# Kernel optimization log

Measured on AMD Instinct MI355X. Metric: run time of the kernel, lower is better.

## Reference

```python
import jax, jax.numpy as jnp
import numpy as np

B, N, CIN, COUT, MAXN, NF, MID = 8, 512, 64, 64, 16, 32, 16
M1 = [3, 32, 32, 1]
M2 = [CIN * COUT, 512, MID]
MR = [CIN * MID, 512, COUT]
BN_EPS = 1e-3  # keras BatchNormalization default epsilon


def mish(v):
    return v * jnp.tanh(jax.nn.softplus(v))


def bn(v, g, b):
    # training-mode batch norm over the row axis (keras BN in learning phase)
    mu = jnp.mean(v, axis=0, keepdims=True)
    var = jnp.var(v, axis=0, keepdims=True)
    return g * (v - mu) * jax.lax.rsqrt(var + BN_EPS) + b


def _mlp(v, layers):
    for W, b, g, be in layers:
        v = bn(mish(v @ W + b), g, be)
    return v


def setup_inputs() -> dict:
    key = jax.random.key(0)
    ks = jax.random.split(key, 16)
    inp = {
        'x': jax.random.normal(ks[0], (B, N, CIN), jnp.float32),
        'xyz': jax.random.normal(ks[1], (B, N, 3), jnp.float32),
        'framepoints': jax.random.normal(ks[2], (NF, 3), jnp.float32),
        'fpw': jax.random.normal(ks[3], (NF, CIN, COUT), jnp.float32) * 0.05,
    }
    ki = 4
    for name, dims in (('m1', M1), ('m2', M2), ('mr', MR)):
        for i in range(len(dims) - 1):
            inp[f'{name}_w{i}'] = jax.random.normal(ks[ki], (dims[i], dims[i + 1]), jnp.float32) / np.float32(np.sqrt(dims[i]))
            inp[f'{name}_b{i}'] = jnp.zeros((dims[i + 1],), jnp.float32)
            inp[f'{name}_g{i}'] = jnp.ones((dims[i + 1],), jnp.float32)
            inp[f'{name}_be{i}'] = jnp.zeros((dims[i + 1],), jnp.float32)
            ki += 1
    return inp


def reference(x, xyz, framepoints, fpw,
              m1_w0, m1_b0, m1_g0, m1_be0,
              m1_w1, m1_b1, m1_g1, m1_be1,
              m1_w2, m1_b2, m1_g2, m1_be2,
              m2_w0, m2_b0, m2_g0, m2_be0,
              m2_w1, m2_b1, m2_g1, m2_be1,
              mr_w0, mr_b0, mr_g0, mr_be0,
              mr_w1, mr_b1, mr_g1, mr_be1):
    Bc, Nc, cin = x.shape
    nf = framepoints.shape[0]
    cout = fpw.shape[2]
    mid = m2_w1.shape[1]

    # pairwise squared distances on FEATURES (as in the original), gram form
    sq = jnp.sum(x * x, axis=-1)  # [B,N]
    d = sq[:, :, None] + sq[:, None, :] - 2.0 * jnp.einsum('bnc,bmc->bnm', x, x)
    _, idx = jax.lax.top_k(-d, MAXN)  # [B,N,maxn] nearest (self first)

    bidx = jnp.arange(Bc)[:, None, None]
    xyz_sl = xyz[bidx, idx]  # [B,N,maxn,3]
    fur = x[bidx, idx]       # [B,N,maxn,cin]

    xyz_sl = xyz_sl.reshape(-1, MAXN, 3)
    rel = (xyz_sl - xyz_sl[:, :1, :]).reshape(-1, 3)  # [B*N*maxn, 3]

    # deterministic random rotation of frame points about the y axis
    ang = jax.random.uniform(jax.random.key(42), ()) * 2.0 * jnp.pi
    c = jnp.cos(ang); s = jnp.sin(ang)
    z = jnp.zeros_like(c); o = jnp.ones_like(c)
    R = jnp.stack([jnp.stack([c, z, s]), jnp.stack([z, o, z]), jnp.stack([-s, z, c])])
    fp = framepoints @ R  # [nf,3]

    sl = jnp.concatenate([rel, fp], axis=0)              # [M+nf, 3]
    diff = (sl[:, None, :] - fp[None, :, :]).reshape(-1, 3)  # [(M+nf)*nf, 3]

    h = _mlp(diff, [(m1_w0, m1_b0, m1_g0, m1_be0),
                    (m1_w1, m1_b1, m1_g1, m1_be1),
                    (m1_w2, m1_b2, m1_g2, m1_be2)])      # [(M+nf)*nf, 1]

    w = _mlp(fpw.reshape(nf, -1), [(m2_w0, m2_b0, m2_g0, m2_be0),
                                   (m2_w1, m2_b1, m2_g1, m2_be1)])  # [nf, mid]

    agg = jnp.sum(h.reshape(-1, nf, 1) * w[None], axis=1)  # [M+nf, mid]
    wmain = agg[:-nf].reshape(-1, MAXN, mid)               # [B*N, maxn, mid]

    f = jnp.einsum('kmc,kmd->kcd', fur.reshape(-1, MAXN, cin), wmain)
    f = f.reshape(-1, cin * mid)
    f = _mlp(f, [(mr_w0, mr_b0, mr_g0, mr_be0),
                 (mr_w1, mr_b1, mr_g1, mr_be1)])           # [B*N, cout]
    return f.reshape(Bc, Nc, cout)
```

## Files before the change

### kernel.cpp

```cpp
#include <hip/hip_runtime.h>
#include <math.h>

#define BB    8
#define NN    512
#define CIN   64
#define MAXN  16
#define NF    32
#define MID   16
#define BN_   4096
#define MSL   65536
#define MTOT  65568
#define RROWS 2098176
#define P2STR 40
#define AST   72

typedef unsigned short ushort_t;
typedef __attribute__((ext_vector_type(8))) short bf16x8;
typedef __attribute__((ext_vector_type(4))) float f32x4;

__device__ __forceinline__ float mishf(float x){
  float t  = __expf(x);
  float u  = 1.0f + t;
  float u2 = u * u;
  float r  = x * (u2 - 1.0f) * __builtin_amdgcn_rcpf(u2 + 1.0f);
  return (x > 15.0f) ? x : r;
}

__device__ __forceinline__ ushort_t f2bf(float f){
  unsigned u = __float_as_uint(f);
  unsigned r = (u + 0x7FFFu + ((u >> 16) & 1u)) >> 16;
  return (ushort_t)r;
}

__device__ __forceinline__ unsigned cvt_pk_bf16(float lo, float hi){
  unsigned r;
  asm("v_cvt_pk_bf16_f32 %0, %1, %2" : "=v"(r) : "v"(lo), "v"(hi));
  return r;
}

__device__ __forceinline__ unsigned rotl32(unsigned v, unsigned s){
  return (v << s) | (v >> (32u - s));
}

__device__ __forceinline__ float jax_uniform42(){
  unsigned ks[3];
  ks[0] = 0u; ks[1] = 42u; ks[2] = 0x1BD11BDAu ^ 0u ^ 42u;
  const unsigned rot[8] = {13u,15u,26u,6u,17u,29u,16u,24u};
  unsigned x0 = ks[0];
  unsigned x1 = ks[1];
  #pragma unroll
  for (int blk = 0; blk < 5; ++blk){
    #pragma unroll
    for (int r = 0; r < 4; ++r){
      x0 += x1;
      x1 = rotl32(x1, rot[(blk & 1) * 4 + r]);
      x1 ^= x0;
    }
    x0 += ks[(blk + 1) % 3];
    x1 += ks[(blk + 2) % 3] + (unsigned)(blk + 1);
  }
  unsigned w = x0 ^ x1;
  return __uint_as_float((w >> 9) | 0x3f800000u) - 1.0f;
}

__global__ __launch_bounds__(256) void k_sq(const float* __restrict__ x, double* __restrict__ sqd){
  int r = blockIdx.x * 256 + threadIdx.x;
  const float4* p = (const float4*)(x + (size_t)r * 64);
  double a0 = 0.0, a1 = 0.0, a2 = 0.0, a3 = 0.0;
  #pragma unroll
  for (int k = 0; k < 16; k += 4){
    float4 v0 = p[k], v1 = p[k+1], v2 = p[k+2], v3 = p[k+3];
    a0 += (double)v0.x*v0.x + (double)v0.y*v0.y + (double)v0.z*v0.z + (double)v0.w*v0.w;
    a1 += (double)v1.x*v1.x + (double)v1.y*v1.y + (double)v1.z*v1.z + (double)v1.w*v1.w;
    a2 += (double)v2.x*v2.x + (double)v2.y*v2.y + (double)v2.z*v2.z + (double)v2.w*v2.w;
    a3 += (double)v3.x*v3.x + (double)v3.y*v3.y + (double)v3.z*v3.z + (double)v3.w*v3.w;
  }
  sqd[r] = (a0 + a1) + (a2 + a3);
}

__global__ __launch_bounds__(256) void k_topk(const float* __restrict__ x, const double* __restrict__ sqd,
                                              int* __restrict__ idxp){
  __shared__ float ct[128 * 65];
  __shared__ float xnl[4][64];
  int tid  = threadIdx.x;
  int lane = tid & 63;
  int wid  = tid >> 6;
  int g = blockIdx.x * 4 + wid;
  int b = g >> 9;
  const float* xb = x + (size_t)b * (NN * CIN);
  {
    int w = tid >> 6, c = tid & 63;
    int nq = (blockIdx.x * 4 + w) & 511;
    xnl[w][c] = xb[nq * 64 + c];
  }
  double sqn = sqd[g];

  double dst[8];
  #pragma unroll 1
  for (int tile = 0; tile < 4; ++tile){
    __syncthreads();
    #pragma unroll
    for (int u = 0; u < 8; ++u){
      int idx = u * 256 + tid;
      int row = idx >> 4, q = idx & 15;
      float4 v = *(const float4*)&xb[(size_t)(tile * 128 + row) * 64 + q * 4];
      float* d = &ct[row * 65 + q * 4];
      d[0] = v.x; d[1] = v.y; d[2] = v.z; d[3] = v.w;
    }
    __syncthreads();
    double a[2][4];
    #pragma unroll
    for (int s = 0; s < 2; ++s)
      #pragma unroll
      for (int i = 0; i < 4; ++i) a[s][i] = 0.0;
    #pragma unroll
    for (int k = 0; k < 16; ++k){
      float4 qv = *(const float4*)&xnl[wid][k * 4];
      double q0 = (double)qv.x, q1 = (double)qv.y, q2 = (double)qv.z, q3 = (double)qv.w;
      #pragma unroll
      for (int s = 0; s < 2; ++s){
        const float* rp = &ct[(lane + 64 * s) * 65 + k * 4];
        a[s][0] += q0 * (double)rp[0];
        a[s][1] += q1 * (double)rp[1];
        a[s][2] += q2 * (double)rp[2];
        a[s][3] += q3 * (double)rp[3];
      }
    }
    #pragma unroll
    for (int s = 0; s < 2; ++s){
      int m = tile * 128 + 64 * s + lane;
      dst[tile * 2 + s] = sqn + sqd[(b << 9) + m] - 2.0 * ((a[s][0] + a[s][1]) + (a[s][2] + a[s][3]));
    }
  }

  for (int it = 0; it < 16; ++it){
    double bd = 1.0e300; int bi = 0x7FFFFFFF;
    #pragma unroll
    for (int j = 0; j < 8; ++j){
      int m = ((j >> 1) << 7) + ((j & 1) << 6) + lane;
      if (dst[j] < bd){ bd = dst[j]; bi = m; }
    }
    #pragma unroll
    for (int off = 1; off < 64; off <<= 1){
      double od = __shfl_xor(bd, off);
      int    oi = __shfl_xor(bi, off);
      if (od < bd || (od == bd && oi < bi)){ bd = od; bi = oi; }
    }
    if (lane == 0) idxp[g * 16 + it] = bi;
    if (lane == (bi & 63)){
      int slot = ((bi >> 7) << 1) | ((bi >> 6) & 1);
      #pragma unroll
      for (int j = 0; j < 8; ++j) if (j == slot) dst[j] = 1.0e300;
    }
  }
}

__global__ __launch_bounds__(256) void k_prep(const float* __restrict__ xyz,
                                              const float* __restrict__ fpts,
                                              const int* __restrict__ idxp,
                                              const float* __restrict__ w0, const float* __restrict__ b0,
                                              float* __restrict__ sib, float* __restrict__ fjt){
  __shared__ float w0l[96], b0l[32];
  int tid = threadIdx.x;
  if (tid < 96) w0l[tid] = w0[tid];
  else if (tid < 128) b0l[tid - 96] = b0[tid - 96];
  __syncthreads();
  int i = blockIdx.x * 256 + tid;
  if (i >= MTOT) return;
  float vx, vy, vz;
  if (i < MSL){
    int bn = i >> 4, m = i & 15, b = bn >> 9;
    int i0 = idxp[bn * 16];
    int im = idxp[bn * 16 + m];
    const float* xz = xyz + (size_t)b * (NN * 3);
    vx = xz[im * 3 + 0] - xz[i0 * 3 + 0];
    vy = xz[im * 3 + 1] - xz[i0 * 3 + 1];
    vz = xz[im * 3 + 2] - xz[i0 * 3 + 2];
  } else {
    int j = i - MSL;
    float u   = jax_uniform42();
    float ang = (u * 2.0f) * 3.14159274f;
    float c = cosf(ang), s = sinf(ang);
    float fx = fpts[j * 3 + 0], fy = fpts[j * 3 + 1], fz = fpts[j * 3 + 2];
    vx = fx * c - fz * s;
    vy = fy;
    vz = fx * s + fz * c;
  }
  float si[32];
  #pragma unroll
  for (int c = 0; c < 32; ++c)
    si[c] = vx * w0l[c] + vy * w0l[32 + c] + vz * w0l[64 + c];
  float* dst = sib + (size_t)i * 32;
  #pragma unroll
  for (int cq = 0; cq < 8; ++cq){
    float4 o = make_float4(si[cq*4+0] + b0l[cq*4+0], si[cq*4+1] + b0l[cq*4+1],
                           si[cq*4+2] + b0l[cq*4+2], si[cq*4+3] + b0l[cq*4+3]);
    *(float4*)&dst[cq*4] = o;
  }
  if (i >= MSL){
    int j = i - MSL;
    #pragma unroll
    for (int c = 0; c < 32; ++c) fjt[c * 32 + j] = si[c];
  }
}

__global__ __launch_bounds__(256) void k_m1_p1(const float* __restrict__ sib, const float* __restrict__ fjt,
                                               float* __restrict__ s0g, float* __restrict__ q0g,
                                               ushort_t* __restrict__ a0g){
  __shared__ float fjlt[32 * 33];
  __shared__ float red[16][32], redq[16][32];
  int tid = threadIdx.x;
  for (int t = tid; t < 1024; t += 256) fjlt[(t & 31) * 33 + (t >> 5)] = fjt[t];
  __syncthreads();
  int c2 = (tid & 15) * 2, s = tid >> 4;
  float as0 = 0.0f, aq0 = 0.0f, as1 = 0.0f, aq1 = 0.0f;
  int base = blockIdx.x * 1024;
  #pragma unroll 4
  for (int t = 0; t < 64; ++t){
    int r = base + t * 16 + s;
    int i = r >> 5, j = r & 31;
    float2 v = *(const float2*)&sib[(size_t)i * 32 + c2];
    float2 f = *(const float2*)&fjlt[j * 33 + c2];
    float m0 = mishf(v.x - f.x);
    float m1 = mishf(v.y - f.y);
    as0 += m0; aq0 += m0 * m0;
    as1 += m1; aq1 += m1 * m1;
    if (a0g) *(unsigned*)&a0g[(size_t)r * 32 + c2] = cvt_pk_bf16(m0, m1);
  }
  red[s][c2] = as0;  red[s][c2 + 1] = as1;
  redq[s][c2] = aq0; redq[s][c2 + 1] = aq1;
  __syncthreads();
  if (tid < 32){
    float ts = 0.0f, tq = 0.0f;
    #pragma unroll
    for (int ss = 0; ss < 16; ++ss){ ts += red[ss][tid]; tq += redq[ss][tid]; }
    int bank = (blockIdx.x & 15) * 32 + tid;
    atomicAdd(&s0g[bank], ts);
    atomicAdd(&q0g[bank], tq);
  }
}

__global__ __launch_bounds__(256, 6) void k_m1_p2(const float* __restrict__ sib, const float* __restrict__ fjt,
                                               const ushort_t* __restrict__ a0g,
                                               const float* __restrict__ w1g, const float* __restrict__ b1g,
                                               const float* __restrict__ g0, const float* __restrict__ be0,
                                               const float* __restrict__ s0g, const float* __restrict__ q0g,
                                               float* __restrict__ s1g, float* __restrict__ q1g,
                                               ushort_t* __restrict__ a1b){
  __shared__ __align__(16) ushort_t a0s[256 * P2STR];
  __shared__ __align__(16) float uni[1024];
  __shared__ float A0l[32], C0l[32], biasX[32], satm[32], qatm[32];
  ushort_t* wts = (ushort_t*)uni;
  int tid = threadIdx.x;
  if (!a0g){
    for (int t = tid; t < 1024; t += 256) uni[t] = fjt[t];
  }
  if (tid < 32){
    float s = 0.0f, q = 0.0f;
    #pragma unroll
    for (int b = 0; b < 16; ++b){ s += s0g[b * 32 + tid]; q += q0g[b * 32 + tid]; }
    const float invR = 1.0f / (float)RROWS;
    float mu = s * invR, var = q * invR - mu * mu;
    float A = g0[tid] * rsqrtf(var + 1e-3f);
    A0l[tid] = A; C0l[tid] = be0[tid] - mu * A;
    satm[tid] = 0.0f; qatm[tid] = 0.0f;
  }
  __syncthreads();
  if (a0g){
    int r = blockIdx.x * 256 + tid;
    const uint4* src = (const uint4*)(a0g + (size_t)r * 32);
    uint4 v0 = src[0], v1 = src[1], v2 = src[2], v3 = src[3];
    ushort_t* dst = &a0s[tid * P2STR];
    *(uint4*)&dst[0]  = v0;
    *(uint4*)&dst[8]  = v1;
    *(uint4*)&dst[16] = v2;
    *(uint4*)&dst[24] = v3;
  } else {
    int r = blockIdx.x * 256 + tid;
    int i = r >> 5, j = r & 31;
    const float* sr = sib + (size_t)i * 32;
    ushort_t* dst = &a0s[tid * P2STR];
    #pragma unroll
    for (int cq = 0; cq < 4; ++cq){
      float4 sa = *(const float4*)&sr[cq * 8];
      float4 sb = *(const float4*)&sr[cq * 8 + 4];
      float m0 = mishf(sa.x - uni[(cq*8+0)*32 + j]);
      float m1 = mishf(sa.y - uni[(cq*8+1)*32 + j]);
      float m2 = mishf(sa.z - uni[(cq*8+2)*32 + j]);
      float m3 = mishf(sa.w - uni[(cq*8+3)*32 + j]);
      float m4 = mishf(sb.x - uni[(cq*8+4)*32 + j]);
      float m5 = mishf(sb.y - uni[(cq*8+5)*32 + j]);
      float m6 = mishf(sb.z - uni[(cq*8+6)*32 + j]);
      float m7 = mishf(sb.w - uni[(cq*8+7)*32 + j]);
      uint4 pk;
      pk.x = cvt_pk_bf16(m0, m1);
      pk.y = cvt_pk_bf16(m2, m3);
      pk.z = cvt_pk_bf16(m4, m5);
      pk.w = cvt_pk_bf16(m6, m7);
      *(uint4*)&dst[cq * 8] = pk;
    }
  }
  if (tid < 32){
    float acc = b1g[tid];
    #pragma unroll
    for (int k = 0; k < 32; ++k) acc += C0l[k] * w1g[k * 32 + tid];
    biasX[tid] = acc;
  }
  __syncthreads();
  for (int t = tid; t < 1024; t += 256){
    int k = t >> 5, c = t & 31;
    wts[c * P2STR + k] = f2bf(w1g[t] * A0l[k]);
  }
  __syncthreads();
  int lane = tid & 63, w = tid >> 6;
  int ln15 = lane & 15, quad = lane >> 4;
  f32x4 zero = {0.0f, 0.0f, 0.0f, 0.0f};
  bf16x8 bfr0 = *(bf16x8*)&wts[(ln15) * P2STR + quad * 8];
  bf16x8 bfr1 = *(bf16x8*)&wts[(16 + ln15) * P2STR + quad * 8];
  f32x4 acc[4][2];
  #pragma unroll
  for (int i2 = 0; i2 < 4; ++i2){
    int row = (w * 4 + i2) * 16 + ln15;
    bf16x8 af = *(bf16x8*)&a0s[row * P2STR + quad * 8];
    acc[i2][0] = __builtin_amdgcn_mfma_f32_16x16x32_bf16(af, bfr0, zero, 0, 0, 0);
    acc[i2][1] = __builtin_amdgcn_mfma_f32_16x16x32_bf16(af, bfr1, zero, 0, 0, 0);
  }
  float cs[2] = {0.0f, 0.0f}, cq2[2] = {0.0f, 0.0f};
  size_t rowbase = (size_t)blockIdx.x * 256 + w * 64 + quad * 4;
  #pragma unroll
  for (int nt = 0; nt < 2; ++nt){
    int col = nt * 16 + ln15;
    float bx = biasX[col];
    size_t colbase = (size_t)col * RROWS;
    #pragma unroll
    for (int i2 = 0; i2 < 4; ++i2){
      f32x4 a = acc[i2][nt];
      float m0 = mishf(a[0] + bx);
      float m1 = mishf(a[1] + bx);
      float m2 = mishf(a[2] + bx);
      float m3 = mishf(a[3] + bx);
      cs[nt]  += m0 + m1 + m2 + m3;
      cq2[nt] += m0*m0 + m1*m1 + m2*m2 + m3*m3;
      if (a1b){
        uint2 pk;
        pk.x = cvt_pk_bf16(m0, m1);
        pk.y = cvt_pk_bf16(m2, m3);
        *(uint2*)&a1b[colbase + rowbase + (size_t)i2 * 16] = pk;
      }
    }
  }
  #pragma unroll
  for (int nt = 0; nt < 2; ++nt){
    float v = cs[nt], u = cq2[nt];
    v += __shfl_xor(v, 16); u += __shfl_xor(u, 16);
    v += __shfl_xor(v, 32); u += __shfl_xor(u, 32);
    if (lane < 16){
      atomicAdd(&satm[nt * 16 + ln15], v);
      atomicAdd(&qatm[nt * 16 + ln15], u);
    }
  }
  __syncthreads();
  if (tid < 32){
    int bank = (blockIdx.x & 15) * 32 + tid;
    atomicAdd(&s1g[bank], satm[tid]);
    atomicAdd(&q1g[bank], qatm[tid]);
  }
}

__global__ __launch_bounds__(256) void k_m1_p3s(const ushort_t* __restrict__ a1b,
                                                const float* __restrict__ w2g, const float* __restrict__ b2g,
                                                const float* __restrict__ g1, const float* __restrict__ be1,
                                                const float* __restrict__ s1g, const float* __restrict__ q1g,
                                                float* __restrict__ act2, float* __restrict__ s2g, float* __restrict__ q2g){
  __shared__ float vvl[32], C1l[32], cb2l[1], r2s[4], r2q[4];
  int tid = threadIdx.x;
  if (tid < 32){
    float s = 0.0f, q = 0.0f;
    #pragma unroll
    for (int b = 0; b < 16; ++b){ s += s1g[b * 32 + tid]; q += q1g[b * 32 + tid]; }
    const float invR = 1.0f / (float)RROWS;
    float mu = s * invR, var = q * invR - mu * mu;
    float A = g1[tid] * rsqrtf(var + 1e-3f);
    C1l[tid] = be1[tid] - mu * A;
    vvl[tid] = A * w2g[tid];
  }
  __syncthreads();
  if (tid == 0){
    float a = b2g[0];
    #pragma unroll
    for (int k = 0; k < 32; ++k) a += C1l[k] * w2g[k];
    cb2l[0] = a;
  }
  __syncthreads();
  size_t r0 = (size_t)blockIdx.x * 512 + (size_t)tid * 2;
  float pre0 = 0.0f, pre1 = 0.0f;
  #pragma unroll
  for (int c = 0; c < 32; ++c){
    unsigned u = *(const unsigned*)&a1b[(size_t)c * RROWS + r0];
    float lo = __uint_as_float(u << 16);
    float hi = __uint_as_float(u & 0xFFFF0000u);
    pre0 += lo * vvl[c];
    pre1 += hi * vvl[c];
  }
  float cb2 = cb2l[0];
  float a20 = mishf(pre0 + cb2);
  float a21 = mishf(pre1 + cb2);
  *(float2*)&act2[r0] = make_float2(a20, a21);
  float ss = a20 + a21, qq = a20*a20 + a21*a21;
  #pragma unroll
  for (int off = 1; off < 64; off <<= 1){ ss += __shfl_xor(ss, off); qq += __shfl_xor(qq, off); }
  int lane = tid & 63, wid = tid >> 6;
  if (lane == 0){ r2s[wid] = ss; r2q[wid] = qq; }
  __syncthreads();
  if (tid == 0){
    atomicAdd(&s2g[blockIdx.x & 15], r2s[0] + r2s[1] + r2s[2] + r2s[3]);
    atomicAdd(&q2g[blockIdx.x & 15], r2q[0] + r2q[1] + r2q[2] + r2q[3]);
  }
}

__global__ __launch_bounds__(256, 3) void k_m1_p3f(const float* __restrict__ sib, const float* __restrict__ fjt,
                                               const float* __restrict__ w1g, const float* __restrict__ b1g,
                                               const float* __restrict__ g0, const float* __restrict__ be0,
                                               const float* __restrict__ g1, const float* __restrict__ be1,
                                               const float* __restrict__ w2g, const float* __restrict__ b2g,
                                               const float* __restrict__ s0g, const float* __restrict__ q0g,
                                               const float* __restrict__ s1g, const float* __restrict__ q1g,
                                               float* __restrict__ act2, float* __restrict__ s2g, float* __restrict__ q2g){
  __shared__ float fjl[1024];
  __shared__ float w1s[1024];
  __shared__ float A0l[32], C0l[32], A1l[32], C1l[32], biasX[32], vvl[32];
  __shared__ float a0t[32 * 256];
  __shared__ float cb2l[1];
  __shared__ float r2s[4], r2q[4];
  int tid = threadIdx.x;
  const float invR = 1.0f / (float)RROWS;
  for (int t = tid; t < 1024; t += 256) fjl[t] = fjt[t];
  if (tid < 32){
    float s = 0.0f, q = 0.0f;
    #pragma unroll
    for (int b = 0; b < 16; ++b){ s += s0g[b * 32 + tid]; q += q0g[b * 32 + tid]; }
    float mu = s * invR, var = q * invR - mu * mu;
    float A = g0[tid] * rsqrtf(var + 1e-3f);
    A0l[tid] = A; C0l[tid] = be0[tid] - mu * A;
  } else if (tid < 64){
    int c = tid - 32;
    float s = 0.0f, q = 0.0f;
    #pragma unroll
    for (int b = 0; b < 16; ++b){ s += s1g[b * 32 + c]; q += q1g[b * 32 + c]; }
    float mu = s * invR, var = q * invR - mu * mu;
    float A = g1[c] * rsqrtf(var + 1e-3f);
    A1l[c] = A; C1l[c] = be1[c] - mu * A;
  }
  __syncthreads();
  for (int t = tid; t < 1024; t += 256) w1s[t] = w1g[t] * A0l[t >> 5];
  if (tid < 32){
    float acc = b1g[tid];
    #pragma unroll
    for (int k = 0; k < 32; ++k) acc += C0l[k] * w1g[k * 32 + tid];
    biasX[tid] = acc;
  } else if (tid < 96 && tid >= 64){
    int c = tid - 64;
    vvl[c] = A1l[c] * w2g[c];
  } else if (tid == 96){
    float acc = b2g[0];
    #pragma unroll
    for (int k = 0; k < 32; ++k) acc += C1l[k] * w2g[k];
    cb2l[0] = acc;
  }
  {
    int r = blockIdx.x * 256 + tid;
    int i = r >> 5, j = r & 31;
    const float* sr = sib + (size_t)i * 32;
    #pragma unroll
    for (int cq = 0; cq < 8; ++cq){
      float4 sv = *(const float4*)&sr[cq * 4];
      a0t[(cq*4+0)*256 + tid] = mishf(sv.x - fjl[(cq*4+0)*32 + j]);
      a0t[(cq*4+1)*256 + tid] = mishf(sv.y - fjl[(cq*4+1)*32 + j]);
      a0t[(cq*4+2)*256 + tid] = mishf(sv.z - fjl[(cq*4+2)*32 + j]);
      a0t[(cq*4+3)*256 + tid] = mishf(sv.w - fjl[(cq*4+3)*32 + j]);
    }
  }
  __syncthreads();
  int cg = tid & 7, rg = tid >> 3;
  float acc[8][4];
  #pragma unroll
  for (int i2 = 0; i2 < 8; ++i2)
    #pragma unroll
    for (int j2 = 0; j2 < 4; ++j2) acc[i2][j2] = 0.0f;
  #pragma unroll 4
  for (int k = 0; k < 32; ++k){
    float4 w  = *(const float4*)&w1s[k * 32 + cg * 4];
    float4 aA = *(const float4*)&a0t[k * 256 + rg * 8];
    float4 aB = *(const float4*)&a0t[k * 256 + rg * 8 + 4];
    float ar[8] = {aA.x, aA.y, aA.z, aA.w, aB.x, aB.y, aB.z, aB.w};
    float wc[4] = {w.x, w.y, w.z, w.w};
    #pragma unroll
    for (int i2 = 0; i2 < 8; ++i2)
      #pragma unroll
      for (int j2 = 0; j2 < 4; ++j2) acc[i2][j2] += ar[i2] * wc[j2];
  }
  float cb2 = cb2l[0];
  float ss = 0.0f, qq = 0.0f;
  #pragma unroll
  for (int rr = 0; rr < 8; ++rr){
    float part = 0.0f;
    #pragma unroll
    for (int cc = 0; cc < 4; ++cc){
      float m = mishf(acc[rr][cc] + biasX[cg * 4 + cc]);
      part += m * vvl[cg * 4 + cc];
    }
    part += __shfl_xor(part, 1);
    part += __shfl_xor(part, 2);
    part += __shfl_xor(part, 4);
    float a2 = mishf(part + cb2);
    if (cg == 0){
      act2[(size_t)blockIdx.x * 256 + rg * 8 + rr] = a2;
      ss += a2; qq += a2 * a2;
    }
  }
  #pragma unroll
  for (int off = 1; off < 64; off <<= 1){ ss += __shfl_xor(ss, off); qq += __shfl_xor(qq, off); }
  int lane = tid & 63, wid = tid >> 6;
  if (lane == 0){ r2s[wid] = ss; r2q[wid] = qq; }
  __syncthreads();
  if (tid == 0){
    atomicAdd(&s2g[blockIdx.x & 15], r2s[0] + r2s[1] + r2s[2] + r2s[3]);
    atomicAdd(&q2g[blockIdx.x & 15], r2q[0] + r2q[1] + r2q[2] + r2q[3]);
  }
}

__global__ __launch_bounds__(512) void k_wmlp1(const float* __restrict__ fpw, const float* __restrict__ W0,
                                               float* __restrict__ wact0){
  int f = blockIdx.x, kc = blockIdx.y, c = threadIdx.x;
  const float* row = fpw + (size_t)f * 4096 + kc * 512;
  const float* wp  = W0 + (size_t)(kc * 512) * 512 + c;
  float acc = 0.0f;
  #pragma unroll 8
  for (int k = 0; k < 512; ++k) acc += row[k] * wp[(size_t)k * 512];
  atomicAdd(&wact0[f * 512 + c], acc);
}

__global__ __launch_bounds__(512) void k_wmlp2(const float* __restrict__ wact0, const float* __restrict__ b0,
                                               const float* __restrict__ W1,
                                               const float* __restrict__ b1,
                                               const float* __restrict__ g0, const float* __restrict__ be0,
                                               const float* __restrict__ g1, const float* __restrict__ be1,
                                               float* __restrict__ wfin){
  __shared__ float wl[32 * 512];
  __shared__ float o2l[512], A1l[16], C1l[16];
  int t = threadIdx.x;
  {
    float b0t = b0[t];
    float v[32]; float sum = 0.0f, sq = 0.0f;
    #pragma unroll
    for (int r = 0; r < 32; ++r){
      v[r] = mishf(wact0[r * 512 + t] + b0t);
      sum += v[r]; sq += v[r] * v[r];
    }
    float mu  = sum * (1.0f / 32.0f);
    float var = sq * (1.0f / 32.0f) - mu * mu;
    float A = g0[t] * rsqrtf(var + 1e-3f);
    float C = be0[t] - mu * A;
    #pragma unroll
    for (int r = 0; r < 32; ++r) wl[r * 512 + t] = v[r] * A + C;
  }
  __syncthreads();
  {
    int r = t >> 4, c2 = t & 15;
    float pre = b1[c2];
    for (int k = 0; k < 512; ++k) pre += wl[r * 512 + k] * W1[k * 16 + c2];
    o2l[t] = mishf(pre);
  }
  __syncthreads();
  if (t < 16){
    float sum = 0.0f, sq = 0.0f;
    #pragma unroll
    for (int r = 0; r < 32; ++r){ float v = o2l[r * 16 + t]; sum += v; sq += v * v; }
    float mu  = sum * (1.0f / 32.0f);
    float var = sq * (1.0f / 32.0f) - mu * mu;
    float A = g1[t] * rsqrtf(var + 1e-3f);
    A1l[t] = A; C1l[t] = be1[t] - mu * A;
  }
  __syncthreads();
  wfin[t] = o2l[t] * A1l[t & 15] + C1l[t & 15];
}

__global__ __launch_bounds__(256) void k_agg(const float* __restrict__ act2, const float* __restrict__ wfin,
                                             const float* __restrict__ x, const int* __restrict__ idxp,
                                             const float* __restrict__ s2, const float* __restrict__ q2,
                                             const float* __restrict__ g2, const float* __restrict__ be2,
                                             ushort_t* __restrict__ fb16){
  __shared__ float hl[512], wfl[512], wm[256], furl[1024], AC[2];
  int t = threadIdx.x;
  int k = blockIdx.x;
  if (t == 0){
    const float invR = 1.0f / (float)RROWS;
    float ssum = 0.0f, qsum = 0.0f;
    #pragma unroll
    for (int b = 0; b < 16; ++b){ ssum += s2[b]; qsum += q2[b]; }
    float mu  = ssum * invR;
    float var = qsum * invR - mu * mu;
    float A = g2[0] * rsqrtf(var + 1e-3f);
    AC[0] = A; AC[1] = be2[0] - mu * A;
  }
  wfl[t] = wfin[t]; wfl[t + 256] = wfin[t + 256];
  __syncthreads();
  float A2 = AC[0], C2 = AC[1];
  hl[t]       = act2[(size_t)k * 512 + t]       * A2 + C2;
  hl[t + 256] = act2[(size_t)k * 512 + 256 + t] * A2 + C2;
  __syncthreads();
  {
    int m = t >> 4, d = t & 15;
    float acc = 0.0f;
    #pragma unroll
    for (int j = 0; j < 32; ++j) acc += hl[m * 32 + j] * wfl[j * 16 + d];
    wm[t] = acc;
  }
  int b = k >> 9;
  const float* xb = x + (size_t)b * (NN * CIN);
  {
    int c = t & 63;
    #pragma unroll
    for (int it = 0; it < 4; ++it){
      int m = it * 4 + (t >> 6);
      int im = idxp[k * 16 + m];
      furl[m * 64 + c] = xb[im * 64 + c];
    }
  }
  __syncthreads();
  {
    int d = t & 15, c0 = t >> 4;
    #pragma unroll
    for (int q = 0; q < 4; ++q){
      int c = c0 + 16 * q;
      float acc = 0.0f;
      #pragma unroll
      for (int m = 0; m < 16; ++m) acc += furl[m * 64 + c] * wm[m * 16 + d];
      fb16[(size_t)k * 1024 + t + 256 * q] = f2bf(acc);
    }
  }
}

__global__ __launch_bounds__(256) void k_mr1(const ushort_t* __restrict__ F16, const float* __restrict__ W,
                                             const float* __restrict__ bias, float* __restrict__ out,
                                             float* __restrict__ s3, float* __restrict__ q3){
  __shared__ __align__(16) ushort_t As[64 * AST];
  __shared__ __align__(16) ushort_t Bs[64 * AST];
  __shared__ float csum[64], csq[64];
  int tid = threadIdx.x;
  int m0 = blockIdx.y * 64, n0 = blockIdx.x * 64;
  int lane = tid & 63, w = tid >> 6;
  int ln15 = lane & 15, quad = lane >> 4;
  if (tid < 64){ csum[tid] = 0.0f; csq[tid] = 0.0f; }
  f32x4 acc[4];
  #pragma unroll
  for (int n = 0; n < 4; ++n){ acc[n][0] = 0.0f; acc[n][1] = 0.0f; acc[n][2] = 0.0f; acc[n][3] = 0.0f; }

  #pragma unroll 1
  for (int k0 = 0; k0 < 1024; k0 += 64){
    __syncthreads();
    {
      int row = tid >> 2, kq = (tid & 3) * 16;
      const uint4* src = (const uint4*)&F16[(size_t)(m0 + row) * 1024 + k0 + kq];
      uint4 v0 = src[0], v1 = src[1];
      ushort_t* dst = &As[row * AST + kq];
      *(uint4*)&dst[0] = v0;
      *(uint4*)&dst[8] = v1;
    }
    #pragma unroll
    for (int rr = 0; rr < 4; ++rr){
      int kk = rr * 16 + (tid >> 4);
      int nn = (tid & 15) * 4;
      float4 v = *(const float4*)&W[(size_t)(k0 + kk) * 512 + n0 + nn];
      unsigned p01 = cvt_pk_bf16(v.x, v.y);
      unsigned p23 = cvt_pk_bf16(v.z, v.w);
      Bs[(nn + 0) * AST + kk] = (ushort_t)p01;
      Bs[(nn + 1) * AST + kk] = (ushort_t)(p01 >> 16);
      Bs[(nn + 2) * AST + kk] = (ushort_t)p23;
      Bs[(nn + 3) * AST + kk] = (ushort_t)(p23 >> 16);
    }
    __syncthreads();
    #pragma unroll
    for (int ks = 0; ks < 64; ks += 32){
      bf16x8 af = *(bf16x8*)&As[(w * 16 + ln15) * AST + ks + quad * 8];
      #pragma unroll
      for (int n = 0; n < 4; ++n){
        bf16x8 bfv = *(bf16x8*)&Bs[(n * 16 + ln15) * AST + ks + quad * 8];
        acc[n] = __builtin_amdgcn_mfma_f32_16x16x32_bf16(af, bfv, acc[n], 0, 0, 0);
      }
    }
  }
  #pragma unroll
  for (int n = 0; n < 4; ++n){
    int col = n0 + n * 16 + ln15;
    float bv = bias[col];
    f32x4 a = acc[n];
    float s = 0.0f, q = 0.0f;
    #pragma unroll
    for (int r = 0; r < 4; ++r){
      float v = mishf(a[r] + bv);
      int row = m0 + w * 16 + quad * 4 + r;
      out[(size_t)row * 512 + col] = v;
      s += v; q += v * v;
    }
    s += __shfl_xor(s, 16); q += __shfl_xor(q, 16);
    s += __shfl_xor(s, 32); q += __shfl_xor(q, 32);
    if (quad == 0){
      atomicAdd(&csum[n * 16 + ln15], s);
      atomicAdd(&csq[n * 16 + ln15], q);
    }
  }
  __syncthreads();
  if (tid < 64){
    atomicAdd(&s3[n0 + tid], csum[tid]);
    atomicAdd(&q3[n0 + tid], csq[tid]);
  }
}

__global__ __launch_bounds__(256) void k_mr2(const float* __restrict__ Ain, const float* __restrict__ W,
                                             const float* __restrict__ bias,
                                             const float* __restrict__ s3, const float* __restrict__ q3,
                                             const float* __restrict__ g0, const float* __restrict__ be0,
                                             float* __restrict__ out, float* __restrict__ s4, float* __restrict__ q4){
  __shared__ float As2[16][68];
  __shared__ float Bs2[16][68];
  __shared__ float A3l[512], C3l[512];
  __shared__ float csum[64], csq[64];
  int tid = threadIdx.x;
  for (int kk = tid; kk < 512; kk += 256){
    const float invR = 1.0f / 4096.0f;
    float mu  = s3[kk] * invR;
    float var = q3[kk] * invR - mu * mu;
    float A = g0[kk] * rsqrtf(var + 1e-3f);
    A3l[kk] = A; C3l[kk] = be0[kk] - mu * A;
  }
  if (tid < 64){ csum[tid] = 0.0f; csq[tid] = 0.0f; }
  __syncthreads();
  int m0 = blockIdx.x * 64;
  int tx = tid & 15, ty = tid >> 4;
  float acc[4][4];
  #pragma unroll
  for (int i = 0; i < 4; ++i)
    #pragma unroll
    for (int j = 0; j < 4; ++j) acc[i][j] = 0.0f;
  int lmm = tid >> 2, lkq = (tid & 3) * 4;
  int lkk = tid >> 4, lnq = (tid & 15) * 4;
  float4 av = *(const float4*)&Ain[(size_t)(m0 + lmm) * 512 + lkq];
  float4 bv = *(const float4*)&W[(size_t)lkk * 64 + lnq];
  for (int k0 = 0; k0 < 512; k0 += 16){
    As2[lkq + 0][lmm] = av.x * A3l[k0 + lkq + 0] + C3l[k0 + lkq + 0];
    As2[lkq + 1][lmm] = av.y * A3l[k0 + lkq + 1] + C3l[k0 + lkq + 1];
    As2[lkq + 2][lmm] = av.z * A3l[k0 + lkq + 2] + C3l[k0 + lkq + 2];
    As2[lkq + 3][lmm] = av.w * A3l[k0 + lkq + 3] + C3l[k0 + lkq + 3];
    *(float4*)&Bs2[lkk][lnq] = bv;
    __syncthreads();
    if (k0 + 16 < 512){
      av = *(const float4*)&Ain[(size_t)(m0 + lmm) * 512 + (k0 + 16) + lkq];
      bv = *(const float4*)&W[(size_t)((k0 + 16) + lkk) * 64 + lnq];
    }
    #pragma unroll
    for (int kk = 0; kk < 16; ++kk){
      float4 a4 = *(const float4*)&As2[kk][ty * 4];
      float4 b4 = *(const float4*)&Bs2[kk][tx * 4];
      float a[4] = {a4.x, a4.y, a4.z, a4.w};
      float bb[4] = {b4.x, b4.y, b4.z, b4.w};
      #pragma unroll
      for (int i = 0; i < 4; ++i)
        #pragma unroll
        for (int j = 0; j < 4; ++j) acc[i][j] += a[i] * bb[j];
    }
    __syncthreads();
  }
  float4 bq = *(const float4*)&bias[tx * 4];
  float bvs[4] = {bq.x, bq.y, bq.z, bq.w};
  float cs[4] = {0,0,0,0}, cq[4] = {0,0,0,0};
  #pragma unroll
  for (int i = 0; i < 4; ++i){
    float v[4];
    #pragma unroll
    for (int j = 0; j < 4; ++j){
      v[j] = mishf(acc[i][j] + bvs[j]);
      cs[j] += v[j]; cq[j] += v[j] * v[j];
    }
    float4 o = make_float4(v[0], v[1], v[2], v[3]);
    *(float4*)&out[(size_t)(m0 + ty * 4 + i) * 64 + tx * 4] = o;
  }
  #pragma unroll
  for (int j = 0; j < 4; ++j){
    float v = cs[j], w = cq[j];
    v += __shfl_xor(v, 16); w += __shfl_xor(w, 16);
    v += __shfl_xor(v, 32); w += __shfl_xor(w, 32);
    if ((tid & 63) < 16){
      atomicAdd(&csum[tx * 4 + j], v);
      atomicAdd(&csq[tx * 4 + j], w);
    }
  }
  __syncthreads();
  if (tid < 64){
    atomicAdd(&s4[tid], csum[tid]);
    atomicAdd(&q4[tid], csq[tid]);
  }
}

__global__ __launch_bounds__(256) void k_out(const float* __restrict__ pre,
                                             const float* __restrict__ s4, const float* __restrict__ q4,
                                             const float* __restrict__ g1, const float* __restrict__ be1,
                                             float* __restrict__ outp){
  int e = blockIdx.x * 256 + threadIdx.x;
  int c = e & 63;
  const float invR = 1.0f / 4096.0f;
  float mu  = s4[c] * invR;
  float var = q4[c] * invR - mu * mu;
  float A = g1[c] * rsqrtf(var + 1e-3f);
  outp[e] = pre[e] * A + (be1[c] - mu * A);
}

extern "C" void kernel_launch(void* const* d_in, const int* in_sizes, int n_in,
                              void* d_out, int out_size, void* d_ws, size_t ws_size,
                              hipStream_t stream){
  (void)in_sizes; (void)n_in; (void)out_size;
  const float* x    = (const float*)d_in[0];
  const float* xyz  = (const float*)d_in[1];
  const float* fpts = (const float*)d_in[2];
  const float* fpw  = (const float*)d_in[3];
  const float* m1w0 = (const float*)d_in[4];
  const float* m1b0 = (const float*)d_in[5];
  const float* m1g0 = (const float*)d_in[6];
  const float* m1be0= (const float*)d_in[7];
  const float* m1w1 = (const float*)d_in[8];
  const float* m1b1 = (const float*)d_in[9];
  const float* m1g1 = (const float*)d_in[10];
  const float* m1be1= (const float*)d_in[11];
  const float* m1w2 = (const float*)d_in[12];
  const float* m1b2 = (const float*)d_in[13];
  const float* m1g2 = (const float*)d_in[14];
  const float* m1be2= (const float*)d_in[15];
  const float* m2w0 = (const float*)d_in[16];
  const float* m2b0 = (const float*)d_in[17];
  const float* m2g0 = (const float*)d_in[18];
  const float* m2be0= (const float*)d_in[19];
  const float* m2w1 = (const float*)d_in[20];
  const float* m2b1 = (const float*)d_in[21];
  const float* m2g1 = (const float*)d_in[22];
  const float* m2be1= (const float*)d_in[23];
  const float* mrw0 = (const float*)d_in[24];
  const float* mrb0 = (const float*)d_in[25];
  const float* mrg0 = (const float*)d_in[26];
  const float* mrbe0= (const float*)d_in[27];
  const float* mrw1 = (const float*)d_in[28];
  const float* mrb1 = (const float*)d_in[29];
  const float* mrg1 = (const float*)d_in[30];
  const float* mrbe1= (const float*)d_in[31];

  float* wsf = (float*)d_ws;
  float* s0 = wsf + 0;     float* q0 = wsf + 512;
  float* s1 = wsf + 1024;  float* q1 = wsf + 1536;
  float* s2 = wsf + 2048;  float* q2 = wsf + 2064;
  float* s3 = wsf + 2080;  float* q3 = wsf + 2592;
  float* s4 = wsf + 3104;  float* q4 = wsf + 3168;
  int*   idxp = (int*)(wsf + 4096);
  double* sqd = (double*)(wsf + 69632);
  float* wact0= wsf + 332032;
  float* wfin = wsf + 348416;
  float* act2 = wsf + 348928;
  float* fbuf = wsf + 2447104;
  float* sib  = fbuf;
  float* fjt  = fbuf + 2098176;
  ushort_t* fb16 = (ushort_t*)fbuf;
  float* mact = wsf + 6641408;
  float* mact2= wsf + 8738560;

  size_t need1 = 9000704ULL * 4 + (size_t)RROWS * 32 * 2;
  size_t need2 = need1 + (size_t)RROWS * 32 * 2;
  bool fast = (ws_size >= need1);
  bool t2   = (ws_size >= need2);
  ushort_t* a1b = fast ? (ushort_t*)(wsf + 9000704) : nullptr;
  ushort_t* a0g = t2   ? (ushort_t*)(wsf + 9000704 + 33570816) : nullptr;

  hipMemsetAsync(d_ws, 0, 4096 * sizeof(float), stream);
  hipMemsetAsync(wact0, 0, 16384 * sizeof(float), stream);

  k_sq<<<16, 256, 0, stream>>>(x, sqd);
  k_topk<<<1024, 256, 0, stream>>>(x, sqd, idxp);
  k_prep<<<257, 256, 0, stream>>>(xyz, fpts, idxp, m1w0, m1b0, sib, fjt);
  k_m1_p1<<<2049, 256, 0, stream>>>(sib, fjt, s0, q0, a0g);
  k_m1_p2<<<8196, 256, 0, stream>>>(sib, fjt, a0g, m1w1, m1b1, m1g0, m1be0, s0, q0, s1, q1, a1b);
  if (fast){
    k_m1_p3s<<<4098, 256, 0, stream>>>(a1b, m1w2, m1b2, m1g1, m1be1, s1, q1, act2, s2, q2);
  } else {
    k_m1_p3f<<<8196, 256, 0, stream>>>(sib, fjt, m1w1, m1b1, m1g0, m1be0, m1g1, m1be1,
                                       m1w2, m1b2, s0, q0, s1, q1, act2, s2, q2);
  }
  k_wmlp1<<<dim3(32, 8), 512, 0, stream>>>(fpw, m2w0, wact0);
  k_wmlp2<<<1, 512, 0, stream>>>(wact0, m2b0, m2w1, m2b1, m2g0, m2be0, m2g1, m2be1, wfin);
  k_agg<<<4096, 256, 0, stream>>>(act2, wfin, x, idxp, s2, q2, m1g2, m1be2, fb16);
  k_mr1<<<dim3(8, 64), 256, 0, stream>>>(fb16, mrw0, mrb0, mact, s3, q3);
  k_mr2<<<64, 256, 0, stream>>>(mact, mrw1, mrb1, s3, q3, mrg0, mrbe0, mact2, s4, q4);
  k_out<<<1024, 256, 0, stream>>>(mact2, s4, q4, mrg1, mrbe1, (float*)d_out);
}
```

Baseline: 466.2 us.

## Restructure m1 layer-2 as direct MFMA, widen p3s loads, pre-convert mr0 weights

Adds a setup kernel that folds the layer-1 batch-norm into bf16 weights and a bias. A new k_m1_p2f kernel then runs layer 2 as MFMAs straight from the global bf16 activations, with no LDS staging. k_m1_p3s now handles 8 rows per thread using 16-byte loads, which cuts its grid fourfold. The mr layer-0 weights are converted to transposed bf16 once, so k_mr1 can read MFMA fragments straight from global memory with no shared tiles or barriers. This adds small extra kernel launches and leans on cache hits for the direct global fragment loads.

```diff
diff --git a/kernel.cpp b/kernel.cpp
--- a/kernel.cpp
+++ b/kernel.cpp
@@ -12,7 +12,6 @@
 #define MTOT  65568
 #define RROWS 2098176
 #define P2STR 40
-#define AST   72
 
 typedef unsigned short ushort_t;
 typedef __attribute__((ext_vector_type(8))) short bf16x8;
@@ -240,8 +239,98 @@
   }
 }
 
+__global__ __launch_bounds__(256) void k_m1_setup(const float* __restrict__ w1g, const float* __restrict__ b1g,
+                                                  const float* __restrict__ g0, const float* __restrict__ be0,
+                                                  const float* __restrict__ s0g, const float* __restrict__ q0g,
+                                                  float* __restrict__ biasXg, ushort_t* __restrict__ wtsb){
+  __shared__ float A0l[32], C0l[32];
+  int tid = threadIdx.x;
+  if (tid < 32){
+    float s = 0.0f, q = 0.0f;
+    #pragma unroll
+    for (int b = 0; b < 16; ++b){ s += s0g[b * 32 + tid]; q += q0g[b * 32 + tid]; }
+    const float invR = 1.0f / (float)RROWS;
+    float mu = s * invR, var = q * invR - mu * mu;
+    float A = g0[tid] * rsqrtf(var + 1e-3f);
+    A0l[tid] = A; C0l[tid] = be0[tid] - mu * A;
+  }
+  __syncthreads();
+  if (tid < 32){
+    float acc = b1g[tid];
+    #pragma unroll
+    for (int k = 0; k < 32; ++k) acc += C0l[k] * w1g[k * 32 + tid];
+    biasXg[tid] = acc;
+  }
+  for (int t = tid; t < 1024; t += 256){
+    int k = t >> 5, c = t & 31;
+    wtsb[c * 32 + k] = f2bf(w1g[t] * A0l[k]);
+  }
+}
+
+__global__ __launch_bounds__(256, 8) void k_m1_p2f(const ushort_t* __restrict__ a0g,
+                                                   const ushort_t* __restrict__ wtsb,
+                                                   const float* __restrict__ biasXg,
+                                                   float* __restrict__ s1g, float* __restrict__ q1g,
+                                                   ushort_t* __restrict__ a1b){
+  __shared__ float satm[32], qatm[32];
+  int tid = threadIdx.x;
+  if (tid < 32){ satm[tid] = 0.0f; qatm[tid] = 0.0f; }
+  __syncthreads();
+  int lane = tid & 63, w = tid >> 6;
+  int ln15 = lane & 15, quad = lane >> 4;
+  bf16x8 bfr0 = *(const bf16x8*)&wtsb[ln15 * 32 + quad * 8];
+  bf16x8 bfr1 = *(const bf16x8*)&wtsb[(16 + ln15) * 32 + quad * 8];
+  f32x4 zero = {0.0f, 0.0f, 0.0f, 0.0f};
+  f32x4 acc[4][2];
+  size_t rowt = (size_t)blockIdx.x * 256;
+  #pragma unroll
+  for (int i2 = 0; i2 < 4; ++i2){
+    int row = (w * 4 + i2) * 16 + ln15;
+    bf16x8 af = *(const bf16x8*)&a0g[(rowt + row) * 32 + quad * 8];
+    acc[i2][0] = __builtin_amdgcn_mfma_f32_16x16x32_bf16(af, bfr0, zero, 0, 0, 0);
+    acc[i2][1] = __builtin_amdgcn_mfma_f32_16x16x32_bf16(af, bfr1, zero, 0, 0, 0);
+  }
+  float cs[2] = {0.0f, 0.0f}, cq2[2] = {0.0f, 0.0f};
+  size_t rowbase = rowt + w * 64 + quad * 4;
+  #pragma unroll
+  for (int nt = 0; nt < 2; ++nt){
+    int col = nt * 16 + ln15;
+    float bx = biasXg[col];
+    size_t colbase = (size_t)col * RROWS;
+    #pragma unroll
+    for (int i2 = 0; i2 < 4; ++i2){
+      f32x4 a = acc[i2][nt];
+      float m0 = mishf(a[0] + bx);
+      float m1 = mishf(a[1] + bx);
+      float m2 = mishf(a[2] + bx);
+      float m3 = mishf(a[3] + bx);
+      cs[nt]  += m0 + m1 + m2 + m3;
+      cq2[nt] += m0*m0 + m1*m1 + m2*m2 + m3*m3;
+      uint2 pk;
+      pk.x = cvt_pk_bf16(m0, m1);
+      pk.y = cvt_pk_bf16(m2, m3);
+      *(uint2*)&a1b[colbase + rowbase + (size_t)i2 * 16] = pk;
+    }
+  }
+  #pragma unroll
+  for (int nt = 0; nt < 2; ++nt){
+    float v = cs[nt], u = cq2[nt];
+    v += __shfl_xor(v, 16); u += __shfl_xor(u, 16);
+    v += __shfl_xor(v, 32); u += __shfl_xor(u, 32);
+    if (lane < 16){
+      atomicAdd(&satm[nt * 16 + ln15], v);
+      atomicAdd(&qatm[nt * 16 + ln15], u);
+    }
+  }
+  __syncthreads();
+  if (tid < 32){
+    int bank = (blockIdx.x & 15) * 32 + tid;
+    atomicAdd(&s1g[bank], satm[tid]);
+    atomicAdd(&q1g[bank], qatm[tid]);
+  }
+}
+
 __global__ __launch_bounds__(256, 6) void k_m1_p2(const float* __restrict__ sib, const float* __restrict__ fjt,
-                                               const ushort_t* __restrict__ a0g,
                                                const float* __restrict__ w1g, const float* __restrict__ b1g,
                                                const float* __restrict__ g0, const float* __restrict__ be0,
                                                const float* __restrict__ s0g, const float* __restrict__ q0g,
@@ -252,9 +341,7 @@
   __shared__ float A0l[32], C0l[32], biasX[32], satm[32], qatm[32];
   ushort_t* wts = (ushort_t*)uni;
   int tid = threadIdx.x;
-  if (!a0g){
-    for (int t = tid; t < 1024; t += 256) uni[t] = fjt[t];
-  }
+  for (int t = tid; t < 1024; t += 256) uni[t] = fjt[t];
   if (tid < 32){
     float s = 0.0f, q = 0.0f;
     #pragma unroll
@@ -266,16 +353,7 @@
     satm[tid] = 0.0f; qatm[tid] = 0.0f;
   }
   __syncthreads();
-  if (a0g){
-    int r = blockIdx.x * 256 + tid;
-    const uint4* src = (const uint4*)(a0g + (size_t)r * 32);
-    uint4 v0 = src[0], v1 = src[1], v2 = src[2], v3 = src[3];
-    ushort_t* dst = &a0s[tid * P2STR];
-    *(uint4*)&dst[0]  = v0;
-    *(uint4*)&dst[8]  = v1;
-    *(uint4*)&dst[16] = v2;
-    *(uint4*)&dst[24] = v3;
-  } else {
+  {
     int r = blockIdx.x * 256 + tid;
     int i = r >> 5, j = r & 31;
     const float* sr = sib + (size_t)i * 32;
@@ -392,21 +470,35 @@
     cb2l[0] = a;
   }
   __syncthreads();
-  size_t r0 = (size_t)blockIdx.x * 512 + (size_t)tid * 2;
-  float pre0 = 0.0f, pre1 = 0.0f;
-  #pragma unroll
-  for (int c = 0; c < 32; ++c){
-    unsigned u = *(const unsigned*)&a1b[(size_t)c * RROWS + r0];
-    float lo = __uint_as_float(u << 16);
-    float hi = __uint_as_float(u & 0xFFFF0000u);
-    pre0 += lo * vvl[c];
-    pre1 += hi * vvl[c];
-  }
-  float cb2 = cb2l[0];
-  float a20 = mishf(pre0 + cb2);
-  float a21 = mishf(pre1 + cb2);
-  *(float2*)&act2[r0] = make_float2(a20, a21);
-  float ss = a20 + a21, qq = a20*a20 + a21*a21;
+  size_t r0 = (size_t)blockIdx.x * 2048 + (size_t)tid * 8;
+  float ss = 0.0f, qq = 0.0f;
+  if (r0 < (size_t)RROWS){
+    float pre[8];
+    #pragma unroll
+    for (int j = 0; j < 8; ++j) pre[j] = 0.0f;
+    #pragma unroll 8
+    for (int c = 0; c < 32; ++c){
+      uint4 u = *(const uint4*)&a1b[(size_t)c * RROWS + r0];
+      float vv = vvl[c];
+      pre[0] += __uint_as_float(u.x << 16) * vv;
+      pre[1] += __uint_as_float(u.x & 0xFFFF0000u) * vv;
+      pre[2] += __uint_as_float(u.y << 16) * vv;
+      pre[3] += __uint_as_float(u.y & 0xFFFF0000u) * vv;
+      pre[4] += __uint_as_float(u.z << 16) * vv;
+      pre[5] += __uint_as_float(u.z & 0xFFFF0000u) * vv;
+      pre[6] += __uint_as_float(u.w << 16) * vv;
+      pre[7] += __uint_as_float(u.w & 0xFFFF0000u) * vv;
+    }
+    float cb2 = cb2l[0];
+    float a2[8];
+    #pragma unroll
+    for (int j = 0; j < 8; ++j){
+      a2[j] = mishf(pre[j] + cb2);
+      ss += a2[j]; qq += a2[j] * a2[j];
+    }
+    *(float4*)&act2[r0]     = make_float4(a2[0], a2[1], a2[2], a2[3]);
+    *(float4*)&act2[r0 + 4] = make_float4(a2[4], a2[5], a2[6], a2[7]);
+  }
   #pragma unroll
   for (int off = 1; off < 64; off <<= 1){ ss += __shfl_xor(ss, off); qq += __shfl_xor(qq, off); }
   int lane = tid & 63, wid = tid >> 6;
@@ -641,54 +733,50 @@
   }
 }
 
-__global__ __launch_bounds__(256) void k_mr1(const ushort_t* __restrict__ F16, const float* __restrict__ W,
+__global__ __launch_bounds__(256) void k_w2bf(const float* __restrict__ W, ushort_t* __restrict__ Wb){
+  int id = blockIdx.x * 256 + threadIdx.x;
+  int n  = id >> 7;
+  int k8 = (id & 127) * 8;
+  float v[8];
+  #pragma unroll
+  for (int j = 0; j < 8; ++j) v[j] = W[(size_t)(k8 + j) * 512 + n];
+  uint4 p;
+  p.x = cvt_pk_bf16(v[0], v[1]);
+  p.y = cvt_pk_bf16(v[2], v[3]);
+  p.z = cvt_pk_bf16(v[4], v[5]);
+  p.w = cvt_pk_bf16(v[6], v[7]);
+  *(uint4*)&Wb[(size_t)n * 1024 + k8] = p;
+}
+
+__global__ __launch_bounds__(256, 8) void k_mr1(const ushort_t* __restrict__ F16, const ushort_t* __restrict__ Wb,
                                              const float* __restrict__ bias, float* __restrict__ out,
                                              float* __restrict__ s3, float* __restrict__ q3){
-  __shared__ __align__(16) ushort_t As[64 * AST];
-  __shared__ __align__(16) ushort_t Bs[64 * AST];
   __shared__ float csum[64], csq[64];
   int tid = threadIdx.x;
   int m0 = blockIdx.y * 64, n0 = blockIdx.x * 64;
   int lane = tid & 63, w = tid >> 6;
   int ln15 = lane & 15, quad = lane >> 4;
   if (tid < 64){ csum[tid] = 0.0f; csq[tid] = 0.0f; }
+  __syncthreads();
   f32x4 acc[4];
   #pragma unroll
   for (int n = 0; n < 4; ++n){ acc[n][0] = 0.0f; acc[n][1] = 0.0f; acc[n][2] = 0.0f; acc[n][3] = 0.0f; }
-
-  #pragma unroll 1
-  for (int k0 = 0; k0 < 1024; k0 += 64){
-    __syncthreads();
-    {
-      int row = tid >> 2, kq = (tid & 3) * 16;
-      const uint4* src = (const uint4*)&F16[(size_t)(m0 + row) * 1024 + k0 + kq];
-      uint4 v0 = src[0], v1 = src[1];
-      ushort_t* dst = &As[row * AST + kq];
-      *(uint4*)&dst[0] = v0;
-      *(uint4*)&dst[8] = v1;
-    }
-    #pragma unroll
-    for (int rr = 0; rr < 4; ++rr){
-      int kk = rr * 16 + (tid >> 4);
-      int nn = (tid & 15) * 4;
-      float4 v = *(const float4*)&W[(size_t)(k0 + kk) * 512 + n0 + nn];
-      unsigned p01 = cvt_pk_bf16(v.x, v.y);
-      unsigned p23 = cvt_pk_bf16(v.z, v.w);
-      Bs[(nn + 0) * AST + kk] = (ushort_t)p01;
-      Bs[(nn + 1) * AST + kk] = (ushort_t)(p01 >> 16);
-      Bs[(nn + 2) * AST + kk] = (ushort_t)p23;
-      Bs[(nn + 3) * AST + kk] = (ushort_t)(p23 >> 16);
-    }
-    __syncthreads();
-    #pragma unroll
-    for (int ks = 0; ks < 64; ks += 32){
-      bf16x8 af = *(bf16x8*)&As[(w * 16 + ln15) * AST + ks + quad * 8];
-      #pragma unroll
-      for (int n = 0; n < 4; ++n){
-        bf16x8 bfv = *(bf16x8*)&Bs[(n * 16 + ln15) * AST + ks + quad * 8];
-        acc[n] = __builtin_amdgcn_mfma_f32_16x16x32_bf16(af, bfv, acc[n], 0, 0, 0);
-      }
-    }
+  const ushort_t* Arow = &F16[(size_t)(m0 + w * 16 + ln15) * 1024 + quad * 8];
+  const ushort_t* B0 = &Wb[(size_t)(n0 +  0 + ln15) * 1024 + quad * 8];
+  const ushort_t* B1 = &Wb[(size_t)(n0 + 16 + ln15) * 1024 + quad * 8];
+  const ushort_t* B2 = &Wb[(size_t)(n0 + 32 + ln15) * 1024 + quad * 8];
+  const ushort_t* B3 = &Wb[(size_t)(n0 + 48 + ln15) * 1024 + quad * 8];
+  #pragma unroll 4
+  for (int k0 = 0; k0 < 1024; k0 += 32){
+    bf16x8 af = *(const bf16x8*)&Arow[k0];
+    bf16x8 b0 = *(const bf16x8*)&B0[k0];
+    bf16x8 b1 = *(const bf16x8*)&B1[k0];
+    bf16x8 b2 = *(const bf16x8*)&B2[k0];
+    bf16x8 b3 = *(const bf16x8*)&B3[k0];
+    acc[0] = __builtin_amdgcn_mfma_f32_16x16x32_bf16(af, b0, acc[0], 0, 0, 0);
+    acc[1] = __builtin_amdgcn_mfma_f32_16x16x32_bf16(af, b1, acc[1], 0, 0, 0);
+    acc[2] = __builtin_amdgcn_mfma_f32_16x16x32_bf16(af, b2, acc[2], 0, 0, 0);
+    acc[3] = __builtin_amdgcn_mfma_f32_16x16x32_bf16(af, b3, acc[3], 0, 0, 0);
   }
   #pragma unroll
   for (int n = 0; n < 4; ++n){
@@ -860,6 +948,8 @@
   float* s4 = wsf + 3104;  float* q4 = wsf + 3168;
   int*   idxp = (int*)(wsf + 4096);
   double* sqd = (double*)(wsf + 69632);
+  float* biasXg = wsf + 77824;
+  ushort_t* wtsb = (ushort_t*)(wsf + 77856);
   float* wact0= wsf + 332032;
   float* wfin = wsf + 348416;
   float* act2 = wsf + 348928;
@@ -867,6 +957,7 @@
   float* sib  = fbuf;
   float* fjt  = fbuf + 2098176;
   ushort_t* fb16 = (ushort_t*)fbuf;
+  ushort_t* wb16 = (ushort_t*)(fbuf + 2099200);
   float* mact = wsf + 6641408;
   float* mact2= wsf + 8738560;
 
@@ -880,13 +971,19 @@
   hipMemsetAsync(d_ws, 0, 4096 * sizeof(float), stream);
   hipMemsetAsync(wact0, 0, 16384 * sizeof(float), stream);
 
+  k_w2bf<<<256, 256, 0, stream>>>(mrw0, wb16);
   k_sq<<<16, 256, 0, stream>>>(x, sqd);
   k_topk<<<1024, 256, 0, stream>>>(x, sqd, idxp);
   k_prep<<<257, 256, 0, stream>>>(xyz, fpts, idxp, m1w0, m1b0, sib, fjt);
   k_m1_p1<<<2049, 256, 0, stream>>>(sib, fjt, s0, q0, a0g);
-  k_m1_p2<<<8196, 256, 0, stream>>>(sib, fjt, a0g, m1w1, m1b1, m1g0, m1be0, s0, q0, s1, q1, a1b);
+  if (t2){
+    k_m1_setup<<<1, 256, 0, stream>>>(m1w1, m1b1, m1g0, m1be0, s0, q0, biasXg, wtsb);
+    k_m1_p2f<<<8196, 256, 0, stream>>>(a0g, wtsb, biasXg, s1, q1, a1b);
+  } else {
+    k_m1_p2<<<8196, 256, 0, stream>>>(sib, fjt, m1w1, m1b1, m1g0, m1be0, s0, q0, s1, q1, a1b);
+  }
   if (fast){
-    k_m1_p3s<<<4098, 256, 0, stream>>>(a1b, m1w2, m1b2, m1g1, m1be1, s1, q1, act2, s2, q2);
+    k_m1_p3s<<<1025, 256, 0, stream>>>(a1b, m1w2, m1b2, m1g1, m1be1, s1, q1, act2, s2, q2);
   } else {
     k_m1_p3f<<<8196, 256, 0, stream>>>(sib, fjt, m1w1, m1b1, m1g0, m1be0, m1g1, m1be1,
                                        m1w2, m1b2, s0, q0, s1, q1, act2, s2, q2);
@@ -894,7 +991,7 @@
   k_wmlp1<<<dim3(32, 8), 512, 0, stream>>>(fpw, m2w0, wact0);
   k_wmlp2<<<1, 512, 0, stream>>>(wact0, m2b0, m2w1, m2b1, m2g0, m2be0, m2g1, m2be1, wfin);
   k_agg<<<4096, 256, 0, stream>>>(act2, wfin, x, idxp, s2, q2, m1g2, m1be2, fb16);
-  k_mr1<<<dim3(8, 64), 256, 0, stream>>>(fb16, mrw0, mrb0, mact, s3, q3);
+  k_mr1<<<dim3(8, 64), 256, 0, stream>>>(fb16, wb16, mrb0, mact, s3, q3);
   k_mr2<<<64, 256, 0, stream>>>(mact, mrw1, mrb1, s3, q3, mrg0, mrbe0, mact2, s4, q4);
   k_out<<<1024, 256, 0, stream>>>(mact2, s4, q4, mrg1, mrbe1, (float*)d_out);
 }
```

Measured after the change: 446.3 us. -4.3%, faster.
